# Kernel tuning notes

Measured on AMD Instinct MI355X. Metric: run time of the kernel, lower is better.

The kernel has to match this reference:

```python
import math
import jax, jax.numpy as jnp
import numpy as np

N, T, C, C2, H, W = 4, 8, 256, 256, 32, 32


def setup_inputs() -> dict:
    key = jax.random.key(0)
    k1, k2, k3 = jax.random.split(key, 3)
    return {
        "key": jax.random.normal(k1, (N, T, C, H, W), dtype=jnp.float32),
        "query": jax.random.normal(k2, (N, T, C, H, W), dtype=jnp.float32),
        "value": jax.random.normal(k3, (N, T, C2, H, W), dtype=jnp.float32),
    }


def reference(key, query, value):
    n, t, c, h, w = key.shape
    c2 = value.shape[2]
    hw = h * w
    k = key.reshape(n, t, c, hw)      # (n,t,c,p)
    q = query.reshape(n, t, c, hw)    # (n,t,c,q)
    v = value.reshape(n, t, c2, hw)   # (n,t,c2,p)
    # scores[p,q] = sum_c K[c,p] * Q[c,q], scaled by sqrt(c)
    scores = jnp.einsum("ntcp,ntcq->ntpq", k, q) / math.sqrt(c)
    # non-standard: softmax over the KEY axis (dim=-2)
    p_attn = jax.nn.softmax(scores, axis=-2)
    # non-standard: V @ attn (contract over key positions p)
    p_val = jnp.einsum("ntcp,ntpq->ntcq", v, p_attn).reshape(n, t, c2, h, w)
    return p_val, p_attn.reshape(n, t, h, w, h, w)
```

## Files before the change

kernel.cpp:

```cpp
#include <hip/hip_runtime.h>
#include <hip/hip_bf16.h>


#define NT_BATCH 32
#define CDIM     256
#define HW       1024

using short8 = __attribute__((ext_vector_type(8))) short;
using f32x16 = __attribute__((ext_vector_type(16))) float;
using f32x4v = __attribute__((ext_vector_type(4))) float;

__device__ __forceinline__ unsigned pk2(float a, float b) {
  float2 t; t.x = a; t.y = b;
  __hip_bfloat162 h = __float22bfloat162_rn(t);
  return *reinterpret_cast<unsigned*>(&h);
}
__device__ __forceinline__ void wr64(void* dst, float a, float b, float c, float d) {
  uint2 v; v.x = pk2(a, b); v.y = pk2(c, d);
  *reinterpret_cast<uint2*>(dst) = v;
}
__device__ __forceinline__ void wr128(void* dst, f32x4v p0, f32x4v p1) {
  uint4 v; v.x = pk2(p0[0], p0[1]); v.y = pk2(p0[2], p0[3]);
  v.z = pk2(p1[0], p1[1]); v.w = pk2(p1[2], p1[3]);
  *reinterpret_cast<uint4*>(dst) = v;
}

__global__ __launch_bounds__(256) void k1_scores(const float* __restrict__ Kp,
                                                 const float* __restrict__ Qp,
                                                 float* __restrict__ E,
                                                 float* __restrict__ colsum) {
  __shared__ __align__(16) unsigned short As[128][40];
  __shared__ __align__(16) unsigned short Bs[128][40];
  __shared__ float csum[128];

  const int nt = blockIdx.y;
  const int pt = blockIdx.x >> 3, qt = blockIdx.x & 7;
  const int p0 = pt * 128, q0 = qt * 128;
  const float* Kb = Kp + (size_t)nt * (CDIM * HW);
  const float* Qb = Qp + (size_t)nt * (CDIM * HW);
  float* Eb = E + (size_t)nt * (HW * HW);

  const int t = threadIdx.x, lane = t & 63;
  const int wave = t >> 6, wm = wave >> 1, wn = wave & 1;
  const int l31 = lane & 31, lhi = lane >> 5;

  const int pblk = ((t & 7) << 2) | ((t >> 3) & 3);
  const int cblk = ((t >> 5) + (t & 7)) & 7;
  const int sp = pblk << 2, sc = cblk << 2;

  if (t < 128) csum[t] = 0.f;

  f32x16 acc[2][2];
  #pragma unroll
  for (int m = 0; m < 2; ++m)
    #pragma unroll
    for (int n = 0; n < 2; ++n)
      #pragma unroll
      for (int r = 0; r < 16; ++r) acc[m][n][r] = 0.f;

  for (int c0 = 0; c0 < CDIM; c0 += 32) {
    f32x4v kv[4], qv[4];
    #pragma unroll
    for (int j = 0; j < 4; ++j) {
      kv[j] = *(const f32x4v*)&Kb[(size_t)(c0 + sc + j) * HW + p0 + sp];
      qv[j] = *(const f32x4v*)&Qb[(size_t)(c0 + sc + j) * HW + q0 + sp];
    }
    __syncthreads();
    #pragma unroll
    for (int i = 0; i < 4; ++i) {
      wr64(&As[sp + i][sc], kv[0][i], kv[1][i], kv[2][i], kv[3][i]);
      wr64(&Bs[sp + i][sc], qv[0][i], qv[1][i], qv[2][i], qv[3][i]);
    }
    __syncthreads();
    #pragma unroll
    for (int ks = 0; ks < 2; ++ks) {
      short8 a[2], b[2];
      #pragma unroll
      for (int m = 0; m < 2; ++m)
        a[m] = *(const short8*)&As[wm * 64 + m * 32 + l31][ks * 16 + lhi * 8];
      #pragma unroll
      for (int n = 0; n < 2; ++n)
        b[n] = *(const short8*)&Bs[wn * 64 + n * 32 + l31][ks * 16 + lhi * 8];
      #pragma unroll
      for (int m = 0; m < 2; ++m)
        #pragma unroll
        for (int n = 0; n < 2; ++n)
          acc[m][n] = __builtin_amdgcn_mfma_f32_32x32x16_bf16(a[m], b[n], acc[m][n], 0, 0, 0);
    }
  }

  float part[2] = {0.f, 0.f};
  #pragma unroll
  for (int m = 0; m < 2; ++m) {
    const int rbase = wm * 64 + m * 32 + (lhi << 2);
    #pragma unroll
    for (int n = 0; n < 2; ++n) {
      const int col = wn * 64 + n * 32 + l31;
      #pragma unroll
      for (int r = 0; r < 16; ++r) {
        int row = rbase + (r & 3) + ((r >> 2) << 3);
        float e = __expf(acc[m][n][r] * 0.0625f);
        Eb[(size_t)(p0 + row) * HW + q0 + col] = e;
        part[n] += e;
      }
    }
  }
  #pragma unroll
  for (int n = 0; n < 2; ++n)
    atomicAdd(&csum[wn * 64 + n * 32 + l31], part[n]);
  __syncthreads();
  if (t < 128) atomicAdd(&colsum[(size_t)nt * HW + q0 + t], csum[t]);
}

__global__ __launch_bounds__(256) void k2_pv(const float* __restrict__ Vp,
                                             float* __restrict__ E,
                                             const float* __restrict__ colsum,
                                             float* __restrict__ O) {
  __shared__ __align__(16) unsigned short Vs[256][72];
  __shared__ __align__(16) unsigned short Ps[64][72];
  __shared__ float inv_s[64];

  const int nt = blockIdx.y, qt = blockIdx.x;
  const int q0 = qt * 64;
  const float* Vb = Vp + (size_t)nt * (CDIM * HW);
  float* Eb = E + (size_t)nt * (HW * HW);
  float* Ob = O + (size_t)nt * (CDIM * HW);

  const int t = threadIdx.x, lane = t & 63, wave = t >> 6;
  const int l31 = lane & 31, lhi = lane >> 5;

  if (t < 64) inv_s[t] = 1.f / colsum[(size_t)nt * HW + q0 + t];

  const int qblk = ((t & 3) << 2) | ((t >> 2) & 3);
  const int pblk = ((t >> 4) + (t & 3)) & 15;
  const int sq = qblk << 2, sp = pblk << 2;
  const int vc = (t >> 2) << 2;
  const int vp = (t & 3) << 4;

  f32x16 acc[2][2];
  #pragma unroll
  for (int m = 0; m < 2; ++m)
    #pragma unroll
    for (int n = 0; n < 2; ++n)
      #pragma unroll
      for (int r = 0; r < 16; ++r) acc[m][n][r] = 0.f;

  __syncthreads();
  const f32x4v inv4 = *(const f32x4v*)&inv_s[sq];

  for (int pb = 0; pb < HW; pb += 64) {
    f32x4v ev[4];
    #pragma unroll
    for (int i = 0; i < 4; ++i)
      ev[i] = *(const f32x4v*)&Eb[(size_t)(pb + sp + i) * HW + q0 + sq];
    f32x4v vv[4][4];
    #pragma unroll
    for (int r = 0; r < 4; ++r)
      #pragma unroll
      for (int g = 0; g < 4; ++g)
        vv[r][g] = *(const f32x4v*)&Vb[(size_t)(vc + r) * HW + pb + vp + (g << 2)];

    #pragma unroll
    for (int i = 0; i < 4; ++i) {
      f32x4v a = ev[i] * inv4;
      *(f32x4v*)&Eb[(size_t)(pb + sp + i) * HW + q0 + sq] = a;
      ev[i] = a;
    }
    __syncthreads();
    #pragma unroll
    for (int j = 0; j < 4; ++j)
      wr64(&Ps[sq + j][sp], ev[0][j], ev[1][j], ev[2][j], ev[3][j]);
    #pragma unroll
    for (int r = 0; r < 4; ++r) {
      wr128(&Vs[vc + r][vp], vv[r][0], vv[r][1]);
      wr128(&Vs[vc + r][vp + 8], vv[r][2], vv[r][3]);
    }
    __syncthreads();
    #pragma unroll
    for (int ks = 0; ks < 4; ++ks) {
      short8 a[2], b[2];
      #pragma unroll
      for (int m = 0; m < 2; ++m)
        a[m] = *(const short8*)&Vs[wave * 64 + m * 32 + l31][ks * 16 + lhi * 8];
      #pragma unroll
      for (int n = 0; n < 2; ++n)
        b[n] = *(const short8*)&Ps[n * 32 + l31][ks * 16 + lhi * 8];
      #pragma unroll
      for (int m = 0; m < 2; ++m)
        #pragma unroll
        for (int n = 0; n < 2; ++n)
          acc[m][n] = __builtin_amdgcn_mfma_f32_32x32x16_bf16(a[m], b[n], acc[m][n], 0, 0, 0);
    }
  }

  #pragma unroll
  for (int m = 0; m < 2; ++m) {
    const int cbase = wave * 64 + m * 32 + (lhi << 2);
    #pragma unroll
    for (int n = 0; n < 2; ++n) {
      const int col = q0 + n * 32 + l31;
      #pragma unroll
      for (int r = 0; r < 16; ++r) {
        int c = cbase + (r & 3) + ((r >> 2) << 3);
        Ob[(size_t)c * HW + col] = acc[m][n][r];
      }
    }
  }
}

extern "C" void kernel_launch(void* const* d_in, const int* in_sizes, int n_in,
                              void* d_out, int out_size, void* d_ws, size_t ws_size,
                              hipStream_t stream) {
  const float* key   = (const float*)d_in[0];
  const float* query = (const float*)d_in[1];
  const float* value = (const float*)d_in[2];
  float* out  = (float*)d_out;
  float* pval = out;
  float* attn = out + (size_t)NT_BATCH * CDIM * HW;
  float* colsum = (float*)d_ws;

  hipMemsetAsync(colsum, 0, (size_t)NT_BATCH * HW * sizeof(float), stream);
  k1_scores<<<dim3(64, NT_BATCH), 256, 0, stream>>>(key, query, attn, colsum);
  k2_pv<<<dim3(16, NT_BATCH), 256, 0, stream>>>(value, attn, colsum, pval);
}
```

Baseline: 360.9 us.

## Recompute scores in PV kernel instead of storing and re-reading unnormalized exp

The first kernel now only computes column sums of exp(scores) and no longer writes the unnormalized attention matrix. The second kernel recomputes the QK^T tile from K and Q, normalizes it, writes the final attention once, and feeds it straight into the V·P matmul through shared memory. This drops a full write plus read-modify-write pass over the 128 MB attention tensor, at the cost of doing the score GEMM twice. It also swizzles the block order so blocks that share a batch run on the same XCD.

```diff
diff --git a/kernel.cpp b/kernel.cpp
--- a/kernel.cpp
+++ b/kernel.cpp
@@ -27,7 +27,6 @@
 
 __global__ __launch_bounds__(256) void k1_scores(const float* __restrict__ Kp,
                                                  const float* __restrict__ Qp,
-                                                 float* __restrict__ E,
                                                  float* __restrict__ colsum) {
   __shared__ __align__(16) unsigned short As[128][40];
   __shared__ __align__(16) unsigned short Bs[128][40];
@@ -38,7 +37,6 @@
   const int p0 = pt * 128, q0 = qt * 128;
   const float* Kb = Kp + (size_t)nt * (CDIM * HW);
   const float* Qb = Qp + (size_t)nt * (CDIM * HW);
-  float* Eb = E + (size_t)nt * (HW * HW);
 
   const int t = threadIdx.x, lane = t & 63;
   const int wave = t >> 6, wm = wave >> 1, wn = wave & 1;
@@ -92,15 +90,11 @@
   float part[2] = {0.f, 0.f};
   #pragma unroll
   for (int m = 0; m < 2; ++m) {
-    const int rbase = wm * 64 + m * 32 + (lhi << 2);
     #pragma unroll
     for (int n = 0; n < 2; ++n) {
-      const int col = wn * 64 + n * 32 + l31;
       #pragma unroll
       for (int r = 0; r < 16; ++r) {
-        int row = rbase + (r & 3) + ((r >> 2) << 3);
         float e = __expf(acc[m][n][r] * 0.0625f);
-        Eb[(size_t)(p0 + row) * HW + q0 + col] = e;
         part[n] += e;
       }
     }
@@ -112,84 +106,126 @@
   if (t < 128) atomicAdd(&colsum[(size_t)nt * HW + q0 + t], csum[t]);
 }
 
-__global__ __launch_bounds__(256) void k2_pv(const float* __restrict__ Vp,
-                                             float* __restrict__ E,
-                                             const float* __restrict__ colsum,
-                                             float* __restrict__ O) {
-  __shared__ __align__(16) unsigned short Vs[256][72];
+__global__ __launch_bounds__(256, 2) void k2_fused(const float* __restrict__ Kp,
+                                                   const float* __restrict__ Qp,
+                                                   const float* __restrict__ Vp,
+                                                   const float* __restrict__ colsum,
+                                                   float* __restrict__ A_out,
+                                                   float* __restrict__ O) {
+  __shared__ __align__(16) unsigned short Qs[64][264];
+  __shared__ __align__(16) unsigned short As[64][72];
+  __shared__ __align__(16) unsigned short Vs[256][40];
   __shared__ __align__(16) unsigned short Ps[64][72];
   __shared__ float inv_s[64];
 
-  const int nt = blockIdx.y, qt = blockIdx.x;
-  const int q0 = qt * 64;
+  const int hbid = blockIdx.y * 16 + blockIdx.x;
+  const int lbid = ((hbid & 7) << 6) | (hbid >> 3);
+  const int nt = lbid >> 4;
+  const int q0 = (lbid & 15) << 6;
+
+  const float* Kb = Kp + (size_t)nt * (CDIM * HW);
+  const float* Qb = Qp + (size_t)nt * (CDIM * HW);
   const float* Vb = Vp + (size_t)nt * (CDIM * HW);
-  float* Eb = E + (size_t)nt * (HW * HW);
+  float* Ab = A_out + (size_t)nt * (HW * HW);
   float* Ob = O + (size_t)nt * (CDIM * HW);
 
-  const int t = threadIdx.x, lane = t & 63, wave = t >> 6;
+  const int t = threadIdx.x, lane = t & 63;
+  const int wave = t >> 6, wm = wave >> 1, wn = wave & 1;
   const int l31 = lane & 31, lhi = lane >> 5;
 
+  const int blkA = ((t & 3) << 2) | ((t >> 2) & 3);
+  const int blkB = ((t >> 4) + (t & 3)) & 15;
+  const int sp = blkA << 2;
+  const int sc = blkB << 2;
+
   if (t < 64) inv_s[t] = 1.f / colsum[(size_t)nt * HW + q0 + t];
 
-  const int qblk = ((t & 3) << 2) | ((t >> 2) & 3);
-  const int pblk = ((t >> 4) + (t & 3)) & 15;
-  const int sq = qblk << 2, sp = pblk << 2;
-  const int vc = (t >> 2) << 2;
-  const int vp = (t & 3) << 4;
-
-  f32x16 acc[2][2];
+  #pragma unroll
+  for (int cc = 0; cc < 4; ++cc) {
+    f32x4v qv[4];
+    #pragma unroll
+    for (int j = 0; j < 4; ++j)
+      qv[j] = *(const f32x4v*)&Qb[(size_t)(cc * 64 + sc + j) * HW + q0 + sp];
+    #pragma unroll
+    for (int i = 0; i < 4; ++i)
+      wr64(&Qs[sp + i][cc * 64 + sc], qv[0][i], qv[1][i], qv[2][i], qv[3][i]);
+  }
+  __syncthreads();
+  const float inv = inv_s[wn * 32 + l31];
+
+  f32x16 accv[2][2];
   #pragma unroll
   for (int m = 0; m < 2; ++m)
     #pragma unroll
     for (int n = 0; n < 2; ++n)
       #pragma unroll
-      for (int r = 0; r < 16; ++r) acc[m][n][r] = 0.f;
-
-  __syncthreads();
-  const f32x4v inv4 = *(const f32x4v*)&inv_s[sq];
-
-  for (int pb = 0; pb < HW; pb += 64) {
-    f32x4v ev[4];
-    #pragma unroll
-    for (int i = 0; i < 4; ++i)
-      ev[i] = *(const f32x4v*)&Eb[(size_t)(pb + sp + i) * HW + q0 + sq];
-    f32x4v vv[4][4];
-    #pragma unroll
-    for (int r = 0; r < 4; ++r)
-      #pragma unroll
-      for (int g = 0; g < 4; ++g)
-        vv[r][g] = *(const f32x4v*)&Vb[(size_t)(vc + r) * HW + pb + vp + (g << 2)];
-
-    #pragma unroll
-    for (int i = 0; i < 4; ++i) {
-      f32x4v a = ev[i] * inv4;
-      *(f32x4v*)&Eb[(size_t)(pb + sp + i) * HW + q0 + sq] = a;
-      ev[i] = a;
-    }
-    __syncthreads();
-    #pragma unroll
-    for (int j = 0; j < 4; ++j)
-      wr64(&Ps[sq + j][sp], ev[0][j], ev[1][j], ev[2][j], ev[3][j]);
-    #pragma unroll
-    for (int r = 0; r < 4; ++r) {
-      wr128(&Vs[vc + r][vp], vv[r][0], vv[r][1]);
-      wr128(&Vs[vc + r][vp + 8], vv[r][2], vv[r][3]);
-    }
-    __syncthreads();
-    #pragma unroll
-    for (int ks = 0; ks < 4; ++ks) {
-      short8 a[2], b[2];
-      #pragma unroll
-      for (int m = 0; m < 2; ++m)
-        a[m] = *(const short8*)&Vs[wave * 64 + m * 32 + l31][ks * 16 + lhi * 8];
-      #pragma unroll
-      for (int n = 0; n < 2; ++n)
-        b[n] = *(const short8*)&Ps[n * 32 + l31][ks * 16 + lhi * 8];
-      #pragma unroll
-      for (int m = 0; m < 2; ++m)
+      for (int r = 0; r < 16; ++r) accv[m][n][r] = 0.f;
+
+  for (int p0 = 0; p0 < HW; p0 += 64) {
+    f32x16 s;
+    #pragma unroll
+    for (int r = 0; r < 16; ++r) s[r] = 0.f;
+
+    for (int c0 = 0; c0 < CDIM; c0 += 64) {
+      f32x4v kv[4];
+      #pragma unroll
+      for (int j = 0; j < 4; ++j)
+        kv[j] = *(const f32x4v*)&Kb[(size_t)(c0 + sc + j) * HW + p0 + sp];
+      __syncthreads();
+      #pragma unroll
+      for (int i = 0; i < 4; ++i)
+        wr64(&As[sp + i][sc], kv[0][i], kv[1][i], kv[2][i], kv[3][i]);
+      __syncthreads();
+      #pragma unroll
+      for (int ks = 0; ks < 4; ++ks) {
+        short8 a = *(const short8*)&As[wm * 32 + l31][ks * 16 + lhi * 8];
+        short8 b = *(const short8*)&Qs[wn * 32 + l31][c0 + ks * 16 + lhi * 8];
+        s = __builtin_amdgcn_mfma_f32_32x32x16_bf16(a, b, s, 0, 0, 0);
+      }
+    }
+
+    float ev[16];
+    #pragma unroll
+    for (int r = 0; r < 16; ++r) ev[r] = __expf(s[r] * 0.0625f) * inv;
+    const int prow = wm * 32 + (lhi << 2);
+    #pragma unroll
+    for (int r = 0; r < 16; ++r) {
+      int row = prow + (r & 3) + ((r >> 2) << 3);
+      Ab[(size_t)(p0 + row) * HW + q0 + wn * 32 + l31] = ev[r];
+    }
+    #pragma unroll
+    for (int rg = 0; rg < 4; ++rg)
+      wr64(&Ps[wn * 32 + l31][wm * 32 + (lhi << 2) + (rg << 3)],
+           ev[4 * rg], ev[4 * rg + 1], ev[4 * rg + 2], ev[4 * rg + 3]);
+
+    #pragma unroll
+    for (int half = 0; half < 2; ++half) {
+      const int ph = p0 + half * 32;
+      const int vrow0 = t >> 1, pc = (t & 1) << 4;
+      f32x4v vv[2][4];
+      #pragma unroll
+      for (int rr = 0; rr < 2; ++rr)
         #pragma unroll
-        for (int n = 0; n < 2; ++n)
-          acc[m][n] = __builtin_amdgcn_mfma_f32_32x32x16_bf16(a[m], b[n], acc[m][n], 0, 0, 0);
+        for (int g = 0; g < 4; ++g)
+          vv[rr][g] = *(const f32x4v*)&Vb[(size_t)((rr << 7) + vrow0) * HW + ph + pc + (g << 2)];
+      __syncthreads();
+      #pragma unroll
+      for (int rr = 0; rr < 2; ++rr) {
+        wr128(&Vs[(rr << 7) + vrow0][pc], vv[rr][0], vv[rr][1]);
+        wr128(&Vs[(rr << 7) + vrow0][pc + 8], vv[rr][2], vv[rr][3]);
+      }
+      __syncthreads();
+      #pragma unroll
+      for (int ks = 0; ks < 2; ++ks) {
+        short8 b0 = *(const short8*)&Ps[l31][half * 32 + ks * 16 + lhi * 8];
+        short8 b1 = *(const short8*)&Ps[32 + l31][half * 32 + ks * 16 + lhi * 8];
+        #pragma unroll
+        for (int m = 0; m < 2; ++m) {
+          short8 a = *(const short8*)&Vs[wave * 64 + m * 32 + l31][ks * 16 + lhi * 8];
+          accv[m][0] = __builtin_amdgcn_mfma_f32_32x32x16_bf16(a, b0, accv[m][0], 0, 0, 0);
+          accv[m][1] = __builtin_amdgcn_mfma_f32_32x32x16_bf16(a, b1, accv[m][1], 0, 0, 0);
+        }
+      }
     }
   }
 
@@ -202,7 +238,7 @@
       #pragma unroll
       for (int r = 0; r < 16; ++r) {
         int c = cbase + (r & 3) + ((r >> 2) << 3);
-        Ob[(size_t)c * HW + col] = acc[m][n][r];
+        Ob[(size_t)c * HW + col] = accv[m][n][r];
       }
     }
   }
@@ -220,6 +256,6 @@
   float* colsum = (float*)d_ws;
 
   hipMemsetAsync(colsum, 0, (size_t)NT_BATCH * HW * sizeof(float), stream);
-  k1_scores<<<dim3(64, NT_BATCH), 256, 0, stream>>>(key, query, attn, colsum);
-  k2_pv<<<dim3(16, NT_BATCH), 256, 0, stream>>>(value, attn, colsum, pval);
-}
+  k1_scores<<<dim3(64, NT_BATCH), 256, 0, stream>>>(key, query, colsum);
+  k2_fused<<<dim3(16, NT_BATCH), 256, 0, stream>>>(key, query, value, colsum, attn, pval);
+}
```

New measurement: 378.7 us. 1.05x slower.

## Fuse score and PV kernels into one per-column-tile kernel

Applied to the files above, without the earlier changes.

Merges the score/exp kernel and the PV kernel into a single kernel in which each block owns a 64-column query tile. The block computes all 1024 key rows for that tile, so the column sums stay in shared memory. This removes the global colsum buffer, the memset and the global atomics. It also adds register prefetching of K, E and V tiles, 512-thread blocks and an XCD-aware block remap. In exchange there are fewer blocks (512), and each block recomputes the K loads for its own tile, so K is re-read per query tile.

```diff
diff --git a/kernel.cpp b/kernel.cpp
--- a/kernel.cpp
+++ b/kernel.cpp
@@ -19,191 +19,181 @@
   uint2 v; v.x = pk2(a, b); v.y = pk2(c, d);
   *reinterpret_cast<uint2*>(dst) = v;
 }
-__device__ __forceinline__ void wr128(void* dst, f32x4v p0, f32x4v p1) {
-  uint4 v; v.x = pk2(p0[0], p0[1]); v.y = pk2(p0[2], p0[3]);
-  v.z = pk2(p1[0], p1[1]); v.w = pk2(p1[2], p1[3]);
-  *reinterpret_cast<uint4*>(dst) = v;
-}
-
-__global__ __launch_bounds__(256) void k1_scores(const float* __restrict__ Kp,
-                                                 const float* __restrict__ Qp,
-                                                 float* __restrict__ E,
-                                                 float* __restrict__ colsum) {
-  __shared__ __align__(16) unsigned short As[128][40];
-  __shared__ __align__(16) unsigned short Bs[128][40];
-  __shared__ float csum[128];
-
-  const int nt = blockIdx.y;
-  const int pt = blockIdx.x >> 3, qt = blockIdx.x & 7;
-  const int p0 = pt * 128, q0 = qt * 128;
+
+union SMEM {
+  struct { unsigned short Qs[64][264]; unsigned short As[256][72]; } a;
+  struct { unsigned short Vs[256][72]; unsigned short Ps[64][72]; } b;
+};
+
+__global__ __launch_bounds__(512, 4) void k_fused(const float* __restrict__ Kp,
+                                                  const float* __restrict__ Qp,
+                                                  const float* __restrict__ Vp,
+                                                  float* __restrict__ A_out,
+                                                  float* __restrict__ O) {
+  __shared__ __align__(16) SMEM sm;
+  __shared__ float csum[64];
+  __shared__ float inv_s[64];
+
+  const int hbid = blockIdx.y * 16 + blockIdx.x;
+  const int lbid = ((hbid & 7) << 6) | (hbid >> 3);
+  const int nt = lbid >> 4;
+  const int q0 = (lbid & 15) << 6;
+
   const float* Kb = Kp + (size_t)nt * (CDIM * HW);
   const float* Qb = Qp + (size_t)nt * (CDIM * HW);
-  float* Eb = E + (size_t)nt * (HW * HW);
+  const float* Vb = Vp + (size_t)nt * (CDIM * HW);
+  float* Ab = A_out + (size_t)nt * (HW * HW);
+  float* Ob = O + (size_t)nt * (CDIM * HW);
 
   const int t = threadIdx.x, lane = t & 63;
-  const int wave = t >> 6, wm = wave >> 1, wn = wave & 1;
+  const int wave = t >> 6;
   const int l31 = lane & 31, lhi = lane >> 5;
 
-  const int pblk = ((t & 7) << 2) | ((t >> 3) & 3);
-  const int cblk = ((t >> 5) + (t & 7)) & 7;
-  const int sp = pblk << 2, sc = cblk << 2;
-
-  if (t < 128) csum[t] = 0.f;
-
-  f32x16 acc[2][2];
+  if (t < 64) csum[t] = 0.f;
+
   #pragma unroll
-  for (int m = 0; m < 2; ++m)
+  for (int j2 = 0; j2 < 2; ++j2) {
+    const int u = t + (j2 << 9);
+    const int cb4 = (u & 63) << 2, qb4 = (u >> 6) << 2;
+    f32x4v qv[4];
+    #pragma unroll
+    for (int j = 0; j < 4; ++j)
+      qv[j] = *(const f32x4v*)&Qb[(size_t)(cb4 + j) * HW + q0 + qb4];
+    #pragma unroll
+    for (int i = 0; i < 4; ++i)
+      wr64(&sm.a.Qs[qb4 + i][cb4], qv[0][i], qv[1][i], qv[2][i], qv[3][i]);
+  }
+
+  f32x4v kreg[2][4];
+  auto loadK = [&](int P0_, int C0_) {
+    #pragma unroll
+    for (int j2 = 0; j2 < 2; ++j2) {
+      const int u = t + (j2 << 9);
+      const int cb = (u & 15) << 2, pp = (u >> 4) << 2;
+      #pragma unroll
+      for (int j = 0; j < 4; ++j)
+        kreg[j2][j] = *(const f32x4v*)&Kb[(size_t)(C0_ + cb + j) * HW + P0_ + pp];
+    }
+  };
+
+  float part[2] = {0.f, 0.f};
+  loadK(0, 0);
+  for (int pt = 0; pt < 4; ++pt) {
+    const int P0 = pt << 8;
+    f32x16 acc[2];
     #pragma unroll
     for (int n = 0; n < 2; ++n)
       #pragma unroll
-      for (int r = 0; r < 16; ++r) acc[m][n][r] = 0.f;
-
-  for (int c0 = 0; c0 < CDIM; c0 += 32) {
-    f32x4v kv[4], qv[4];
-    #pragma unroll
-    for (int j = 0; j < 4; ++j) {
-      kv[j] = *(const f32x4v*)&Kb[(size_t)(c0 + sc + j) * HW + p0 + sp];
-      qv[j] = *(const f32x4v*)&Qb[(size_t)(c0 + sc + j) * HW + q0 + sp];
-    }
-    __syncthreads();
-    #pragma unroll
-    for (int i = 0; i < 4; ++i) {
-      wr64(&As[sp + i][sc], kv[0][i], kv[1][i], kv[2][i], kv[3][i]);
-      wr64(&Bs[sp + i][sc], qv[0][i], qv[1][i], qv[2][i], qv[3][i]);
-    }
-    __syncthreads();
-    #pragma unroll
-    for (int ks = 0; ks < 2; ++ks) {
-      short8 a[2], b[2];
-      #pragma unroll
-      for (int m = 0; m < 2; ++m)
-        a[m] = *(const short8*)&As[wm * 64 + m * 32 + l31][ks * 16 + lhi * 8];
-      #pragma unroll
-      for (int n = 0; n < 2; ++n)
-        b[n] = *(const short8*)&Bs[wn * 64 + n * 32 + l31][ks * 16 + lhi * 8];
-      #pragma unroll
-      for (int m = 0; m < 2; ++m)
+      for (int r = 0; r < 16; ++r) acc[n][r] = 0.f;
+
+    #pragma unroll
+    for (int cc = 0; cc < 4; ++cc) {
+      __syncthreads();
+      #pragma unroll
+      for (int j2 = 0; j2 < 2; ++j2) {
+        const int u = t + (j2 << 9);
+        const int cb = (u & 15) << 2, pp = (u >> 4) << 2;
         #pragma unroll
-        for (int n = 0; n < 2; ++n)
-          acc[m][n] = __builtin_amdgcn_mfma_f32_32x32x16_bf16(a[m], b[n], acc[m][n], 0, 0, 0);
-    }
-  }
-
-  float part[2] = {0.f, 0.f};
-  #pragma unroll
-  for (int m = 0; m < 2; ++m) {
-    const int rbase = wm * 64 + m * 32 + (lhi << 2);
+        for (int i = 0; i < 4; ++i)
+          wr64(&sm.a.As[pp + i][cb],
+               kreg[j2][0][i], kreg[j2][1][i], kreg[j2][2][i], kreg[j2][3][i]);
+      }
+      if (cc < 3) loadK(P0, (cc + 1) << 6);
+      else if (pt < 3) loadK(P0 + 256, 0);
+      __syncthreads();
+      #pragma unroll
+      for (int ks = 0; ks < 4; ++ks) {
+        short8 a_ = *(const short8*)&sm.a.As[wave * 32 + l31][ks * 16 + lhi * 8];
+        short8 b0 = *(const short8*)&sm.a.Qs[l31][(cc << 6) + ks * 16 + lhi * 8];
+        short8 b1 = *(const short8*)&sm.a.Qs[32 + l31][(cc << 6) + ks * 16 + lhi * 8];
+        acc[0] = __builtin_amdgcn_mfma_f32_32x32x16_bf16(a_, b0, acc[0], 0, 0, 0);
+        acc[1] = __builtin_amdgcn_mfma_f32_32x32x16_bf16(a_, b1, acc[1], 0, 0, 0);
+      }
+    }
+
+    const int rbase = wave * 32 + (lhi << 2);
     #pragma unroll
     for (int n = 0; n < 2; ++n) {
-      const int col = wn * 64 + n * 32 + l31;
+      const int col = q0 + n * 32 + l31;
       #pragma unroll
       for (int r = 0; r < 16; ++r) {
-        int row = rbase + (r & 3) + ((r >> 2) << 3);
-        float e = __expf(acc[m][n][r] * 0.0625f);
-        Eb[(size_t)(p0 + row) * HW + q0 + col] = e;
+        float e = __expf(acc[n][r] * 0.0625f);
         part[n] += e;
+        const int row = P0 + rbase + (r & 3) + ((r >> 2) << 3);
+        Ab[(size_t)row * HW + col] = e;
       }
     }
   }
+
+  atomicAdd(&csum[l31], part[0]);
+  atomicAdd(&csum[32 + l31], part[1]);
+  __syncthreads();
+  if (t < 64) inv_s[t] = 1.0f / csum[t];
+  __syncthreads();
+
+  const int pr2 = t >> 4;
+  const int sq = (t & 15) << 2;
+  const f32x4v inv4 = *(const f32x4v*)&inv_s[sq];
+  const int vc = t >> 1, vp = (t & 1) << 5;
+
+  f32x4v er[2];
+  f32x4v vreg[8];
+  auto loadE = [&](int pb_) {
+    er[0] = *(const f32x4v*)&Ab[(size_t)(pb_ + 2 * pr2) * HW + q0 + sq];
+    er[1] = *(const f32x4v*)&Ab[(size_t)(pb_ + 2 * pr2 + 1) * HW + q0 + sq];
+  };
+  auto loadV = [&](int pb_) {
+    #pragma unroll
+    for (int g = 0; g < 8; ++g)
+      vreg[g] = *(const f32x4v*)&Vb[(size_t)vc * HW + pb_ + vp + (g << 2)];
+  };
+
+  f32x16 av[2];
   #pragma unroll
   for (int n = 0; n < 2; ++n)
-    atomicAdd(&csum[wn * 64 + n * 32 + l31], part[n]);
-  __syncthreads();
-  if (t < 128) atomicAdd(&colsum[(size_t)nt * HW + q0 + t], csum[t]);
-}
-
-__global__ __launch_bounds__(256) void k2_pv(const float* __restrict__ Vp,
-                                             float* __restrict__ E,
-                                             const float* __restrict__ colsum,
-                                             float* __restrict__ O) {
-  __shared__ __align__(16) unsigned short Vs[256][72];
-  __shared__ __align__(16) unsigned short Ps[64][72];
-  __shared__ float inv_s[64];
-
-  const int nt = blockIdx.y, qt = blockIdx.x;
-  const int q0 = qt * 64;
-  const float* Vb = Vp + (size_t)nt * (CDIM * HW);
-  float* Eb = E + (size_t)nt * (HW * HW);
-  float* Ob = O + (size_t)nt * (CDIM * HW);
-
-  const int t = threadIdx.x, lane = t & 63, wave = t >> 6;
-  const int l31 = lane & 31, lhi = lane >> 5;
-
-  if (t < 64) inv_s[t] = 1.f / colsum[(size_t)nt * HW + q0 + t];
-
-  const int qblk = ((t & 3) << 2) | ((t >> 2) & 3);
-  const int pblk = ((t >> 4) + (t & 3)) & 15;
-  const int sq = qblk << 2, sp = pblk << 2;
-  const int vc = (t >> 2) << 2;
-  const int vp = (t & 3) << 4;
-
-  f32x16 acc[2][2];
+    #pragma unroll
+    for (int r = 0; r < 16; ++r) av[n][r] = 0.f;
+
+  loadE(0); loadV(0);
+  for (int tile = 0; tile < 16; ++tile) {
+    const int pb = tile << 6;
+    const f32x4v a0 = er[0] * inv4;
+    const f32x4v a1 = er[1] * inv4;
+    __syncthreads();
+    #pragma unroll
+    for (int j = 0; j < 4; ++j)
+      *reinterpret_cast<unsigned*>(&sm.b.Ps[sq + j][2 * pr2]) = pk2(a0[j], a1[j]);
+    #pragma unroll
+    for (int g = 0; g < 4; ++g) {
+      uint4 w_;
+      w_.x = pk2(vreg[2 * g][0], vreg[2 * g][1]);
+      w_.y = pk2(vreg[2 * g][2], vreg[2 * g][3]);
+      w_.z = pk2(vreg[2 * g + 1][0], vreg[2 * g + 1][1]);
+      w_.w = pk2(vreg[2 * g + 1][2], vreg[2 * g + 1][3]);
+      *reinterpret_cast<uint4*>(&sm.b.Vs[vc][vp + (g << 3)]) = w_;
+    }
+    if (tile < 15) { loadE(pb + 64); loadV(pb + 64); }
+    *(f32x4v*)&Ab[(size_t)(pb + 2 * pr2) * HW + q0 + sq] = a0;
+    *(f32x4v*)&Ab[(size_t)(pb + 2 * pr2 + 1) * HW + q0 + sq] = a1;
+    __syncthreads();
+    #pragma unroll
+    for (int kk = 0; kk < 4; ++kk) {
+      short8 a_ = *(const short8*)&sm.b.Vs[wave * 32 + l31][kk * 16 + lhi * 8];
+      short8 b0 = *(const short8*)&sm.b.Ps[l31][kk * 16 + lhi * 8];
+      short8 b1 = *(const short8*)&sm.b.Ps[32 + l31][kk * 16 + lhi * 8];
+      av[0] = __builtin_amdgcn_mfma_f32_32x32x16_bf16(a_, b0, av[0], 0, 0, 0);
+      av[1] = __builtin_amdgcn_mfma_f32_32x32x16_bf16(a_, b1, av[1], 0, 0, 0);
+    }
+  }
+
   #pragma unroll
-  for (int m = 0; m < 2; ++m)
-    #pragma unroll
-    for (int n = 0; n < 2; ++n)
-      #pragma unroll
-      for (int r = 0; r < 16; ++r) acc[m][n][r] = 0.f;
-
-  __syncthreads();
-  const f32x4v inv4 = *(const f32x4v*)&inv_s[sq];
-
-  for (int pb = 0; pb < HW; pb += 64) {
-    f32x4v ev[4];
-    #pragma unroll
-    for (int i = 0; i < 4; ++i)
-      ev[i] = *(const f32x4v*)&Eb[(size_t)(pb + sp + i) * HW + q0 + sq];
-    f32x4v vv[4][4];
-    #pragma unroll
-    for (int r = 0; r < 4; ++r)
-      #pragma unroll
-      for (int g = 0; g < 4; ++g)
-        vv[r][g] = *(const f32x4v*)&Vb[(size_t)(vc + r) * HW + pb + vp + (g << 2)];
-
-    #pragma unroll
-    for (int i = 0; i < 4; ++i) {
-      f32x4v a = ev[i] * inv4;
-      *(f32x4v*)&Eb[(size_t)(pb + sp + i) * HW + q0 + sq] = a;
-      ev[i] = a;
-    }
-    __syncthreads();
-    #pragma unroll
-    for (int j = 0; j < 4; ++j)
-      wr64(&Ps[sq + j][sp], ev[0][j], ev[1][j], ev[2][j], ev[3][j]);
-    #pragma unroll
-    for (int r = 0; r < 4; ++r) {
-      wr128(&Vs[vc + r][vp], vv[r][0], vv[r][1]);
-      wr128(&Vs[vc + r][vp + 8], vv[r][2], vv[r][3]);
-    }
-    __syncthreads();
-    #pragma unroll
-    for (int ks = 0; ks < 4; ++ks) {
-      short8 a[2], b[2];
-      #pragma unroll
-      for (int m = 0; m < 2; ++m)
-        a[m] = *(const short8*)&Vs[wave * 64 + m * 32 + l31][ks * 16 + lhi * 8];
-      #pragma unroll
-      for (int n = 0; n < 2; ++n)
-        b[n] = *(const short8*)&Ps[n * 32 + l31][ks * 16 + lhi * 8];
-      #pragma unroll
-      for (int m = 0; m < 2; ++m)
-        #pragma unroll
-        for (int n = 0; n < 2; ++n)
-          acc[m][n] = __builtin_amdgcn_mfma_f32_32x32x16_bf16(a[m], b[n], acc[m][n], 0, 0, 0);
-    }
-  }
-
-  #pragma unroll
-  for (int m = 0; m < 2; ++m) {
-    const int cbase = wave * 64 + m * 32 + (lhi << 2);
-    #pragma unroll
-    for (int n = 0; n < 2; ++n) {
-      const int col = q0 + n * 32 + l31;
-      #pragma unroll
-      for (int r = 0; r < 16; ++r) {
-        int c = cbase + (r & 3) + ((r >> 2) << 3);
-        Ob[(size_t)c * HW + col] = acc[m][n][r];
-      }
+  for (int n = 0; n < 2; ++n) {
+    const int col = q0 + n * 32 + l31;
+    const int cbase = wave * 32 + (lhi << 2);
+    #pragma unroll
+    for (int r = 0; r < 16; ++r) {
+      const int c = cbase + (r & 3) + ((r >> 2) << 3);
+      Ob[(size_t)c * HW + col] = av[n][r];
     }
   }
 }
@@ -217,9 +207,6 @@
   float* out  = (float*)d_out;
   float* pval = out;
   float* attn = out + (size_t)NT_BATCH * CDIM * HW;
-  float* colsum = (float*)d_ws;
-
-  hipMemsetAsync(colsum, 0, (size_t)NT_BATCH * HW * sizeof(float), stream);
-  k1_scores<<<dim3(64, NT_BATCH), 256, 0, stream>>>(key, query, attn, colsum);
-  k2_pv<<<dim3(16, NT_BATCH), 256, 0, stream>>>(value, attn, colsum, pval);
-}
+
+  k_fused<<<dim3(16, NT_BATCH), 512, 0, stream>>>(key, query, value, attn, pval);
+}
```

Result: slower. 420.4 us (+16.5%).
